# Kernel tuning notes

Measured on AMD Instinct MI355X. Metric: run time of the kernel, lower is better.

The kernel has to match this reference:

```python
import jax, jax.numpy as jnp
import numpy as np

NUM_HEAD = 8
HEAD_DIM = 64
TEMPERATURE = 10000.0


def positional_encoding(L, D):
    # Mirrors get_positional_encoding: sin on even-indexed, cos on odd-indexed
    # columns of pos, interleaved via stack+reshape.
    embed = jnp.arange(L, dtype=jnp.float32)
    dim_t = jnp.arange(D, dtype=jnp.float32)
    dim_t = TEMPERATURE ** (2.0 * jnp.floor(dim_t / 2.0) / D)
    pos = embed[:, None] / dim_t                      # [L, D]
    pos = jnp.stack([jnp.sin(pos[:, 0::2]), jnp.cos(pos[:, 1::2])], axis=2)
    return pos.reshape(1, L, D)                       # [1, L, D]


def setup_inputs() -> dict:
    key = jax.random.key(0)
    ks = jax.random.split(key, 4)
    B, L, D = 8, 1024, 256
    HD = NUM_HEAD * HEAD_DIM                          # 512
    glorot = float(np.sqrt(2.0 / (D + HD)))
    return {
        "x": jax.random.normal(ks[0], (B, L, D), jnp.float32),
        "Wq": jax.random.normal(ks[1], (D, HD), jnp.float32) * glorot,
        "bq": jnp.zeros((NUM_HEAD,), jnp.float32),
        "Wk": jax.random.normal(ks[2], (D, HD), jnp.float32) * glorot,
        "bk": jnp.zeros((NUM_HEAD,), jnp.float32),
        "Wv": jax.random.normal(ks[3], (D, HD), jnp.float32) * glorot,
        "bv": jnp.zeros((NUM_HEAD,), jnp.float32),
    }


def reference(x, Wq, bq, Wk, bk, Wv, bv):
    B, L, D = x.shape
    pe = positional_encoding(L, D)
    qk_in = x + pe                                    # query/key get pos-enc, value does not
    # per-head bias broadcast over head_dim (tf.repeat(bias, head_dim))
    q = qk_in @ Wq + jnp.repeat(bq, HEAD_DIM)
    k = qk_in @ Wk + jnp.repeat(bk, HEAD_DIM)
    v = x @ Wv + jnp.repeat(bv, HEAD_DIM)
    split = lambda t: t.reshape(B, L, NUM_HEAD, HEAD_DIM)
    q, k, v = split(q), split(k), split(v)
    att = jnp.einsum('blhd,bmhd->bhlm', q, k) * (float(HEAD_DIM) ** -0.5)
    att = jax.nn.softmax(att, axis=-1)                # [B, H, L, L]
    out = jnp.einsum('bhlm,bmhd->blhd', att, v)       # [B, L, H, hd]
    return out.reshape(B, L, NUM_HEAD * HEAD_DIM)
```

## Files before the change

kernel.cpp:

```cpp
#include <hip/hip_runtime.h>
#include <hip/hip_bf16.h>

#define NB   8
#define NL   1024
#define ND   256
#define NH   8
#define NHD  64
#define NC   512
#define NTOK (NB*NL)

typedef __bf16 bf16x8v __attribute__((ext_vector_type(8)));
typedef float f32x4 __attribute__((ext_vector_type(4)));

__device__ __forceinline__ unsigned short f2bf(float f) {
  unsigned u = __float_as_uint(f);
  unsigned r = (u + 0x7fffu + ((u >> 16) & 1u)) >> 16;
  return (unsigned short)r;
}

__device__ __forceinline__ unsigned pack_bf16x2(float lo, float hi) {
  __hip_bfloat162 h2 = __float22bfloat162_rn(make_float2(lo, hi));
  union { __hip_bfloat162 h; unsigned u; } cvt;
  cvt.h = h2;
  return cvt.u;
}

__global__ __launch_bounds__(256) void prep_kernel(
    const float* __restrict__ x,
    const float* __restrict__ Wq, const float* __restrict__ Wk,
    const float* __restrict__ Wv,
    unsigned short* __restrict__ xpe, unsigned short* __restrict__ xb,
    unsigned short* __restrict__ wqt, unsigned short* __restrict__ wkt,
    unsigned short* __restrict__ wvt) {
  const int bid = blockIdx.x;
  const int tid = threadIdx.x;
  if (bid < (NTOK * ND) / (256 * 8)) {
    int idx = bid * 256 + tid;
    int d0 = (idx & 31) * 8;
    int t = idx >> 5;
    int l = t & (NL - 1);
    float4 xa = *(const float4*)(x + (size_t)t * ND + d0);
    float4 xc = *(const float4*)(x + (size_t)t * ND + d0 + 4);
    float xv[8] = {xa.x, xa.y, xa.z, xa.w, xc.x, xc.y, xc.z, xc.w};
    unsigned short pe_out[8], xb_out[8];
#pragma unroll
    for (int p = 0; p < 4; ++p) {
      float inv_dim = __expf(-0.07195578415606394f * (float)(d0 / 2 + p));
      float ang = (float)l * inv_dim;
      float sv = __sinf(ang);
      float cv = __cosf(ang);
      pe_out[2 * p]     = f2bf(xv[2 * p] + sv);
      pe_out[2 * p + 1] = f2bf(xv[2 * p + 1] + cv);
      xb_out[2 * p]     = f2bf(xv[2 * p]);
      xb_out[2 * p + 1] = f2bf(xv[2 * p + 1]);
    }
    *(int4*)(xpe + (size_t)t * ND + d0) = *(int4*)pe_out;
    *(int4*)(xb  + (size_t)t * ND + d0) = *(int4*)xb_out;
  } else {
    __shared__ float tile[64 * 65];
    int widx = bid - (NTOK * ND) / (256 * 8);
    int m = widx >> 5;
    int tl = widx & 31;
    int kt = tl & 3;
    int nt = tl >> 2;
    const float* W = (m == 0) ? Wq : (m == 1) ? Wk : Wv;
    unsigned short* Wt = (m == 0) ? wqt : (m == 1) ? wkt : wvt;
    int c = tid & 63, rb = tid >> 6;
#pragma unroll
    for (int i = 0; i < 16; ++i) {
      int r = i * 4 + rb;
      tile[r * 65 + c] = W[(kt * 64 + r) * NC + nt * 64 + c];
    }
    __syncthreads();
#pragma unroll
    for (int i = 0; i < 16; ++i) {
      int n_local = i * 4 + rb, k_local = c;
      Wt[(nt * 64 + n_local) * ND + kt * 64 + k_local] =
          f2bf(tile[k_local * 65 + n_local]);
    }
  }
}

__global__ __launch_bounds__(256) void gemm_qkv_kernel(
    const unsigned short* __restrict__ xpe, const unsigned short* __restrict__ xb,
    const unsigned short* __restrict__ wqt, const unsigned short* __restrict__ wkt,
    const unsigned short* __restrict__ wvt,
    const float* __restrict__ bq, const float* __restrict__ bk,
    const float* __restrict__ bv,
    unsigned short* __restrict__ qg, unsigned short* __restrict__ kg,
    unsigned short* __restrict__ vg) {
  __shared__ unsigned short As[128 * 72];
  __shared__ unsigned short Bs[128 * 72];

  const int z = blockIdx.z;
  const unsigned short* X  = (z == 2) ? xb : xpe;
  const unsigned short* Wt = (z == 0) ? wqt : (z == 1) ? wkt : wvt;
  const float* bias        = (z == 0) ? bq  : (z == 1) ? bk  : bv;
  unsigned short* Out      = (z == 0) ? qg  : (z == 1) ? kg  : vg;
  const float scale        = (z == 0) ? 0.18033688011112042f : 1.0f;

  const int nt = blockIdx.x;
  const int mt = blockIdx.y;
  const int tid = threadIdx.x;
  const int w = tid >> 6;
  const int wm = w >> 1, wn = w & 1;
  const int lane = tid & 63;
  const int lg = lane >> 4;
  const int lr = lane & 15;

  const int r0 = tid >> 3;
  const int c8o = (tid & 7) * 8;
  const unsigned short* Abase = X + (size_t)(mt * 128 + r0) * ND + c8o;
  const unsigned short* Bbase = Wt + (size_t)(nt * 128 + r0) * ND + c8o;
  unsigned short* Adst = As + r0 * 72 + c8o;
  unsigned short* Bdst = Bs + r0 * 72 + c8o;

  f32x4 acc[4][4] = {};
  int4 a0, a1, a2, a3, b0, b1, b2, b3;

#define GLOADS(kb)                                              \
  a0 = *(const int4*)(Abase + (kb) * 64);                       \
  a1 = *(const int4*)(Abase + (kb) * 64 + 32 * ND);             \
  a2 = *(const int4*)(Abase + (kb) * 64 + 64 * ND);             \
  a3 = *(const int4*)(Abase + (kb) * 64 + 96 * ND);             \
  b0 = *(const int4*)(Bbase + (kb) * 64);                       \
  b1 = *(const int4*)(Bbase + (kb) * 64 + 32 * ND);             \
  b2 = *(const int4*)(Bbase + (kb) * 64 + 64 * ND);             \
  b3 = *(const int4*)(Bbase + (kb) * 64 + 96 * ND);

  GLOADS(0)
#pragma unroll
  for (int kb = 0; kb < 4; ++kb) {
    if (kb) __syncthreads();
    *(int4*)(Adst)           = a0;
    *(int4*)(Adst + 32 * 72) = a1;
    *(int4*)(Adst + 64 * 72) = a2;
    *(int4*)(Adst + 96 * 72) = a3;
    *(int4*)(Bdst)           = b0;
    *(int4*)(Bdst + 32 * 72) = b1;
    *(int4*)(Bdst + 64 * 72) = b2;
    *(int4*)(Bdst + 96 * 72) = b3;
    if (kb == 0) { GLOADS(1) }
    else if (kb == 1) { GLOADS(2) }
    else if (kb == 2) { GLOADS(3) }
    __syncthreads();

#pragma unroll
    for (int kk = 0; kk < 2; ++kk) {
      bf16x8v a[4], b[4];
#pragma unroll
      for (int mi = 0; mi < 4; ++mi)
        a[mi] = *(const bf16x8v*)(As + (wm * 64 + mi * 16 + lr) * 72 + kk * 32 + lg * 8);
#pragma unroll
      for (int nj = 0; nj < 4; ++nj)
        b[nj] = *(const bf16x8v*)(Bs + (wn * 64 + nj * 16 + lr) * 72 + kk * 32 + lg * 8);
#pragma unroll
      for (int mi = 0; mi < 4; ++mi)
#pragma unroll
        for (int nj = 0; nj < 4; ++nj)
          acc[mi][nj] = __builtin_amdgcn_mfma_f32_16x16x32_bf16(
              a[mi], b[nj], acc[mi][nj], 0, 0, 0);
    }
  }
#undef GLOADS

  const float bval = bias[nt * 2 + wn];
  const int h = nt * 2 + wn;
#pragma unroll
  for (int mi = 0; mi < 4; ++mi) {
#pragma unroll
    for (int nj = 0; nj < 4; ++nj) {
#pragma unroll
      for (int j = 0; j < 4; ++j) {
        int r = mt * 128 + wm * 64 + mi * 16 + lg * 4 + j;
        int dd = nj * 16 + lr;
        int bb = r >> 10, lpos = r & (NL - 1);
        float val = (acc[mi][nj][j] + bval) * scale;
        if (z < 2)
          Out[((bb * NH + h) * NL + lpos) * NHD + dd] = f2bf(val);
        else
          Out[((bb * NH + h) * NHD + dd) * NL + lpos] = f2bf(val);
      }
    }
  }
}

__global__ __launch_bounds__(256) void attn_kernel(
    const unsigned short* __restrict__ Q,
    const unsigned short* __restrict__ K,
    const unsigned short* __restrict__ Vt,
    float* __restrict__ Out) {
  __shared__ unsigned short Ks[64 * 72];
  __shared__ unsigned short Vs[64 * 72];
  __shared__ unsigned short Ps[64 * 72];

  const int qt = blockIdx.x;
  const int bh = blockIdx.y;
  const int bb = bh >> 3, h = bh & 7;
  const int tid = threadIdx.x;
  const int w = tid >> 6;
  const int lane = tid & 63;
  const int lg = lane >> 4, lr = lane & 15;
  const int qrow0 = qt * 64 + w * 16;

  bf16x8v qf[2];
#pragma unroll
  for (int kk = 0; kk < 2; ++kk)
    qf[kk] = *(const bf16x8v*)(Q + ((size_t)bh * NL + qrow0 + lr) * NHD + kk * 32 + lg * 8);

  const int r0 = tid >> 3;
  const int c8o = (tid & 7) * 8;
  const unsigned short* kp0 = K + (size_t)bh * NL * NHD + r0 * NHD + c8o;
  const unsigned short* vp0 = Vt + ((size_t)bh * NHD + r0) * NL + c8o;
  unsigned short* kdst = Ks + r0 * 72 + c8o;
  unsigned short* vdst = Vs + r0 * 72 + c8o;

  float m_ = -1e30f, lsum = 0.0f;
  f32x4 o[4] = {};
  int4 ka, kc, va, vc;

#define KVLOADS(kv)                                             \
  ka = *(const int4*)(kp0 + (kv) * 64 * NHD);                   \
  kc = *(const int4*)(kp0 + (kv) * 64 * NHD + 32 * NHD);        \
  va = *(const int4*)(vp0 + (kv) * 64);                         \
  vc = *(const int4*)(vp0 + (kv) * 64 + 32 * NL);

  KVLOADS(0)
  for (int kv = 0; kv < 16; ++kv) {
    if (kv) __syncthreads();
    *(int4*)(kdst)           = ka;
    *(int4*)(kdst + 32 * 72) = kc;
    *(int4*)(vdst)           = va;
    *(int4*)(vdst + 32 * 72) = vc;
    if (kv < 15) { KVLOADS(kv + 1) }
    __syncthreads();

    f32x4 s[4] = {};
    __builtin_amdgcn_s_setprio(1);
#pragma unroll
    for (int kk = 0; kk < 2; ++kk) {
#pragma unroll
      for (int nb = 0; nb < 4; ++nb) {
        bf16x8v kf = *(const bf16x8v*)(Ks + (nb * 16 + lr) * 72 + kk * 32 + lg * 8);
        s[nb] = __builtin_amdgcn_mfma_f32_16x16x32_bf16(kf, qf[kk], s[nb], 0, 0, 0);
      }
    }
    __builtin_amdgcn_s_setprio(0);

    float tm;
    {
      float a0 = fmaxf(s[0][0], s[0][1]), a1 = fmaxf(s[0][2], s[0][3]);
      float a2 = fmaxf(s[1][0], s[1][1]), a3 = fmaxf(s[1][2], s[1][3]);
      float a4 = fmaxf(s[2][0], s[2][1]), a5 = fmaxf(s[2][2], s[2][3]);
      float a6 = fmaxf(s[3][0], s[3][1]), a7 = fmaxf(s[3][2], s[3][3]);
      float c0 = fmaxf(fmaxf(a0, a1), fmaxf(a2, a3));
      float c1 = fmaxf(fmaxf(a4, a5), fmaxf(a6, a7));
      tm = fmaxf(c0, c1);
    }
    tm = fmaxf(tm, __shfl_xor(tm, 16, 64));
    tm = fmaxf(tm, __shfl_xor(tm, 32, 64));
    if (__any(tm > m_ + 8.0f)) {
      float nm = fmaxf(m_, tm);
      float corr = exp2f(m_ - nm);
      m_ = nm;
      lsum *= corr;
#pragma unroll
      for (int db = 0; db < 4; ++db)
#pragma unroll
        for (int j = 0; j < 4; ++j) o[db][j] *= corr;
    }
#pragma unroll
    for (int nb = 0; nb < 4; ++nb)
#pragma unroll
      for (int j = 0; j < 4; ++j)
        s[nb][j] = exp2f(s[nb][j] - m_);
    float ts;
    {
      float a0 = s[0][0] + s[0][1], a1 = s[0][2] + s[0][3];
      float a2 = s[1][0] + s[1][1], a3 = s[1][2] + s[1][3];
      float a4 = s[2][0] + s[2][1], a5 = s[2][2] + s[2][3];
      float a6 = s[3][0] + s[3][1], a7 = s[3][2] + s[3][3];
      ts = ((a0 + a1) + (a2 + a3)) + ((a4 + a5) + (a6 + a7));
    }
    ts += __shfl_xor(ts, 16, 64);
    ts += __shfl_xor(ts, 32, 64);
    lsum += ts;

#pragma unroll
    for (int nb = 0; nb < 4; ++nb)
#pragma unroll
      for (int hh = 0; hh < 2; ++hh)
        *(unsigned*)(Ps + (w * 16 + lr) * 72 + nb * 16 + lg * 4 + 2 * hh) =
            pack_bf16x2(s[nb][2 * hh], s[nb][2 * hh + 1]);

    __builtin_amdgcn_s_setprio(1);
#pragma unroll
    for (int kk = 0; kk < 2; ++kk) {
      bf16x8v pf = *(const bf16x8v*)(Ps + (w * 16 + lr) * 72 + kk * 32 + lg * 8);
#pragma unroll
      for (int db = 0; db < 4; ++db) {
        bf16x8v vf = *(const bf16x8v*)(Vs + (db * 16 + lr) * 72 + kk * 32 + lg * 8);
        o[db] = __builtin_amdgcn_mfma_f32_16x16x32_bf16(vf, pf, o[db], 0, 0, 0);
      }
    }
    __builtin_amdgcn_s_setprio(0);
  }
#undef KVLOADS

  float inv = 1.0f / lsum;
  int q = qrow0 + lr;
#pragma unroll
  for (int db = 0; db < 4; ++db) {
    f32x4 ov;
#pragma unroll
    for (int j = 0; j < 4; ++j) ov[j] = o[db][j] * inv;
    *(f32x4*)(Out + (size_t)(bb * NL + q) * NC + h * NHD + db * 16 + lg * 4) = ov;
  }
}

extern "C" void kernel_launch(void* const* d_in, const int* in_sizes, int n_in,
                              void* d_out, int out_size, void* d_ws, size_t ws_size,
                              hipStream_t stream) {
  const float* x  = (const float*)d_in[0];
  const float* Wq = (const float*)d_in[1];
  const float* bq = (const float*)d_in[2];
  const float* Wk = (const float*)d_in[3];
  const float* bk = (const float*)d_in[4];
  const float* Wv = (const float*)d_in[5];
  const float* bv = (const float*)d_in[6];
  float* out = (float*)d_out;

  unsigned short* xpe = (unsigned short*)d_ws;
  unsigned short* xb  = xpe + (size_t)NTOK * ND;
  unsigned short* wqt = xb  + (size_t)NTOK * ND;
  unsigned short* wkt = wqt + (size_t)ND * NC;
  unsigned short* wvt = wkt + (size_t)ND * NC;
  unsigned short* qg  = wvt + (size_t)ND * NC;
  unsigned short* kg  = qg  + (size_t)NB * NH * NL * NHD;
  unsigned short* vg  = kg  + (size_t)NB * NH * NL * NHD;

  int prep_blocks = (NTOK * ND) / (256 * 8) + 96;
  prep_kernel<<<prep_blocks, 256, 0, stream>>>(x, Wq, Wk, Wv, xpe, xb, wqt, wkt, wvt);

  gemm_qkv_kernel<<<dim3(4, 64, 3), 256, 0, stream>>>(
      xpe, xb, wqt, wkt, wvt, bq, bk, bv, qg, kg, vg);

  attn_kernel<<<dim3(16, 64), 256, 0, stream>>>(qg, kg, vg, out);
}
```

Before: 137.9 us.

## Fuse input conversion, positional encoding and weight transpose into QKV GEMM

Removes the separate prep kernel. The QKV GEMM now reads fp32 x and W directly, adds the sin/cos positional encoding on the fly for Q and K, converts to bf16, and transposes the weight tile into shared memory itself. This drops one launch and the bf16 intermediate round trip through global memory. In exchange the GEMM loses its register prefetch of the next k-block, recomputes the PE transcendentals in every N-tile block, and reads fp32 data at twice the width. The change also XOR-swizzles the LDS layouts of As, Bs, Ks, Vs and Ps to reduce bank conflicts.

After: 134.5 us. 1.03x faster.

```diff
diff --git a/kernel.cpp b/kernel.cpp
--- a/kernel.cpp
+++ b/kernel.cpp
@@ -25,66 +25,10 @@
   return cvt.u;
 }
 
-__global__ __launch_bounds__(256) void prep_kernel(
+__global__ __launch_bounds__(256) void gemm_qkv_fused_kernel(
     const float* __restrict__ x,
     const float* __restrict__ Wq, const float* __restrict__ Wk,
     const float* __restrict__ Wv,
-    unsigned short* __restrict__ xpe, unsigned short* __restrict__ xb,
-    unsigned short* __restrict__ wqt, unsigned short* __restrict__ wkt,
-    unsigned short* __restrict__ wvt) {
-  const int bid = blockIdx.x;
-  const int tid = threadIdx.x;
-  if (bid < (NTOK * ND) / (256 * 8)) {
-    int idx = bid * 256 + tid;
-    int d0 = (idx & 31) * 8;
-    int t = idx >> 5;
-    int l = t & (NL - 1);
-    float4 xa = *(const float4*)(x + (size_t)t * ND + d0);
-    float4 xc = *(const float4*)(x + (size_t)t * ND + d0 + 4);
-    float xv[8] = {xa.x, xa.y, xa.z, xa.w, xc.x, xc.y, xc.z, xc.w};
-    unsigned short pe_out[8], xb_out[8];
-#pragma unroll
-    for (int p = 0; p < 4; ++p) {
-      float inv_dim = __expf(-0.07195578415606394f * (float)(d0 / 2 + p));
-      float ang = (float)l * inv_dim;
-      float sv = __sinf(ang);
-      float cv = __cosf(ang);
-      pe_out[2 * p]     = f2bf(xv[2 * p] + sv);
-      pe_out[2 * p + 1] = f2bf(xv[2 * p + 1] + cv);
-      xb_out[2 * p]     = f2bf(xv[2 * p]);
-      xb_out[2 * p + 1] = f2bf(xv[2 * p + 1]);
-    }
-    *(int4*)(xpe + (size_t)t * ND + d0) = *(int4*)pe_out;
-    *(int4*)(xb  + (size_t)t * ND + d0) = *(int4*)xb_out;
-  } else {
-    __shared__ float tile[64 * 65];
-    int widx = bid - (NTOK * ND) / (256 * 8);
-    int m = widx >> 5;
-    int tl = widx & 31;
-    int kt = tl & 3;
-    int nt = tl >> 2;
-    const float* W = (m == 0) ? Wq : (m == 1) ? Wk : Wv;
-    unsigned short* Wt = (m == 0) ? wqt : (m == 1) ? wkt : wvt;
-    int c = tid & 63, rb = tid >> 6;
-#pragma unroll
-    for (int i = 0; i < 16; ++i) {
-      int r = i * 4 + rb;
-      tile[r * 65 + c] = W[(kt * 64 + r) * NC + nt * 64 + c];
-    }
-    __syncthreads();
-#pragma unroll
-    for (int i = 0; i < 16; ++i) {
-      int n_local = i * 4 + rb, k_local = c;
-      Wt[(nt * 64 + n_local) * ND + kt * 64 + k_local] =
-          f2bf(tile[k_local * 65 + n_local]);
-    }
-  }
-}
-
-__global__ __launch_bounds__(256) void gemm_qkv_kernel(
-    const unsigned short* __restrict__ xpe, const unsigned short* __restrict__ xb,
-    const unsigned short* __restrict__ wqt, const unsigned short* __restrict__ wkt,
-    const unsigned short* __restrict__ wvt,
     const float* __restrict__ bq, const float* __restrict__ bk,
     const float* __restrict__ bv,
     unsigned short* __restrict__ qg, unsigned short* __restrict__ kg,
@@ -93,11 +37,11 @@
   __shared__ unsigned short Bs[128 * 72];
 
   const int z = blockIdx.z;
-  const unsigned short* X  = (z == 2) ? xb : xpe;
-  const unsigned short* Wt = (z == 0) ? wqt : (z == 1) ? wkt : wvt;
-  const float* bias        = (z == 0) ? bq  : (z == 1) ? bk  : bv;
-  unsigned short* Out      = (z == 0) ? qg  : (z == 1) ? kg  : vg;
-  const float scale        = (z == 0) ? 0.18033688011112042f : 1.0f;
+  const float* Wsrc = (z == 0) ? Wq : (z == 1) ? Wk : Wv;
+  const float* bias = (z == 0) ? bq : (z == 1) ? bk : bv;
+  unsigned short* Out = (z == 0) ? qg : (z == 1) ? kg : vg;
+  const float scale = (z == 0) ? 0.18033688011112042f : 1.0f;
+  const bool addpe = (z < 2);
 
   const int nt = blockIdx.x;
   const int mt = blockIdx.y;
@@ -105,55 +49,83 @@
   const int w = tid >> 6;
   const int wm = w >> 1, wn = w & 1;
   const int lane = tid & 63;
-  const int lg = lane >> 4;
-  const int lr = lane & 15;
-
-  const int r0 = tid >> 3;
-  const int c8o = (tid & 7) * 8;
-  const unsigned short* Abase = X + (size_t)(mt * 128 + r0) * ND + c8o;
-  const unsigned short* Bbase = Wt + (size_t)(nt * 128 + r0) * ND + c8o;
-  unsigned short* Adst = As + r0 * 72 + c8o;
-  unsigned short* Bdst = Bs + r0 * 72 + c8o;
+  const int lg = lane >> 4, lr = lane & 15;
+
+  const int r0 = tid >> 3, c8 = tid & 7;
+  unsigned short* Adst = As + r0 * 72 + 8 * ((c8 + 2 * (r0 & 7)) & 7);
+  const float* xbase = x + (size_t)(mt * 128 + r0) * ND + c8 * 8;
+  const int no = tid & 15, kp0 = tid >> 4;
 
   f32x4 acc[4][4] = {};
-  int4 a0, a1, a2, a3, b0, b1, b2, b3;
-
-#define GLOADS(kb)                                              \
-  a0 = *(const int4*)(Abase + (kb) * 64);                       \
-  a1 = *(const int4*)(Abase + (kb) * 64 + 32 * ND);             \
-  a2 = *(const int4*)(Abase + (kb) * 64 + 64 * ND);             \
-  a3 = *(const int4*)(Abase + (kb) * 64 + 96 * ND);             \
-  b0 = *(const int4*)(Bbase + (kb) * 64);                       \
-  b1 = *(const int4*)(Bbase + (kb) * 64 + 32 * ND);             \
-  b2 = *(const int4*)(Bbase + (kb) * 64 + 64 * ND);             \
-  b3 = *(const int4*)(Bbase + (kb) * 64 + 96 * ND);
-
-  GLOADS(0)
-#pragma unroll
+
   for (int kb = 0; kb < 4; ++kb) {
     if (kb) __syncthreads();
-    *(int4*)(Adst)           = a0;
-    *(int4*)(Adst + 32 * 72) = a1;
-    *(int4*)(Adst + 64 * 72) = a2;
-    *(int4*)(Adst + 96 * 72) = a3;
-    *(int4*)(Bdst)           = b0;
-    *(int4*)(Bdst + 32 * 72) = b1;
-    *(int4*)(Bdst + 64 * 72) = b2;
-    *(int4*)(Bdst + 96 * 72) = b3;
-    if (kb == 0) { GLOADS(1) }
-    else if (kb == 1) { GLOADS(2) }
-    else if (kb == 2) { GLOADS(3) }
+    float i0 = 0.f, i1 = 0.f, i2 = 0.f, i3 = 0.f;
+    if (addpe) {
+      int dh = kb * 32 + c8 * 4;
+      i0 = __expf(-0.07195578415606394f * (float)(dh));
+      i1 = __expf(-0.07195578415606394f * (float)(dh + 1));
+      i2 = __expf(-0.07195578415606394f * (float)(dh + 2));
+      i3 = __expf(-0.07195578415606394f * (float)(dh + 3));
+    }
+#pragma unroll
+    for (int i = 0; i < 4; ++i) {
+      int row = r0 + 32 * i;
+      f32x4 xa = *(const f32x4*)(xbase + (size_t)(32 * i) * ND + kb * 64);
+      f32x4 xc = *(const f32x4*)(xbase + (size_t)(32 * i) * ND + kb * 64 + 4);
+      unsigned p0, p1, p2, p3;
+      if (addpe) {
+        float l = (float)((mt * 128 + row) & (NL - 1));
+        float a0 = l * i0, a1 = l * i1, a2 = l * i2, a3 = l * i3;
+        p0 = pack_bf16x2(xa[0] + __sinf(a0), xa[1] + __cosf(a0));
+        p1 = pack_bf16x2(xa[2] + __sinf(a1), xa[3] + __cosf(a1));
+        p2 = pack_bf16x2(xc[0] + __sinf(a2), xc[1] + __cosf(a2));
+        p3 = pack_bf16x2(xc[2] + __sinf(a3), xc[3] + __cosf(a3));
+      } else {
+        p0 = pack_bf16x2(xa[0], xa[1]);
+        p1 = pack_bf16x2(xa[2], xa[3]);
+        p2 = pack_bf16x2(xc[0], xc[1]);
+        p3 = pack_bf16x2(xc[2], xc[3]);
+      }
+      int4 pv; pv.x = (int)p0; pv.y = (int)p1; pv.z = (int)p2; pv.w = (int)p3;
+      *(int4*)(Adst + (size_t)(32 * i) * 72) = pv;
+    }
+#pragma unroll
+    for (int u = 0; u < 2; ++u) {
+      int kp = kp0 + 16 * u;
+      int krow = kb * 64 + 2 * kp;
+      const float* wr0 = Wsrc + (size_t)krow * NC + nt * 128 + no * 8;
+      const float* wr1 = wr0 + NC;
+      f32x4 w0a = *(const f32x4*)(wr0);
+      f32x4 w0b = *(const f32x4*)(wr0 + 4);
+      f32x4 w1a = *(const f32x4*)(wr1);
+      f32x4 w1b = *(const f32x4*)(wr1 + 4);
+#pragma unroll
+      for (int e = 0; e < 8; ++e) {
+        float lo = (e < 4) ? w0a[e] : w0b[e - 4];
+        float hi = (e < 4) ? w1a[e] : w1b[e - 4];
+        int n = no * 8 + e;
+        *(unsigned*)(Bs + n * 72 + 8 * (((kp >> 2) + (no & 7)) & 7) +
+                     (kp & 3) * 2) = pack_bf16x2(lo, hi);
+      }
+    }
     __syncthreads();
 
 #pragma unroll
     for (int kk = 0; kk < 2; ++kk) {
       bf16x8v a[4], b[4];
 #pragma unroll
-      for (int mi = 0; mi < 4; ++mi)
-        a[mi] = *(const bf16x8v*)(As + (wm * 64 + mi * 16 + lr) * 72 + kk * 32 + lg * 8);
-#pragma unroll
-      for (int nj = 0; nj < 4; ++nj)
-        b[nj] = *(const bf16x8v*)(Bs + (wn * 64 + nj * 16 + lr) * 72 + kk * 32 + lg * 8);
+      for (int mi = 0; mi < 4; ++mi) {
+        int row = wm * 64 + mi * 16 + lr;
+        a[mi] = *(const bf16x8v*)(As + row * 72 +
+                                  8 * ((4 * kk + lg + 2 * (row & 7)) & 7));
+      }
+#pragma unroll
+      for (int nj = 0; nj < 4; ++nj) {
+        int n = wn * 64 + nj * 16 + lr;
+        b[nj] = *(const bf16x8v*)(Bs + n * 72 +
+                                  8 * ((4 * kk + lg + ((n >> 3) & 7)) & 7));
+      }
 #pragma unroll
       for (int mi = 0; mi < 4; ++mi)
 #pragma unroll
@@ -162,7 +134,6 @@
               a[mi], b[nj], acc[mi][nj], 0, 0, 0);
     }
   }
-#undef GLOADS
 
   const float bval = bias[nt * 2 + wn];
   const int h = nt * 2 + wn;
@@ -209,11 +180,12 @@
     qf[kk] = *(const bf16x8v*)(Q + ((size_t)bh * NL + qrow0 + lr) * NHD + kk * 32 + lg * 8);
 
   const int r0 = tid >> 3;
-  const int c8o = (tid & 7) * 8;
-  const unsigned short* kp0 = K + (size_t)bh * NL * NHD + r0 * NHD + c8o;
-  const unsigned short* vp0 = Vt + ((size_t)bh * NHD + r0) * NL + c8o;
-  unsigned short* kdst = Ks + r0 * 72 + c8o;
-  unsigned short* vdst = Vs + r0 * 72 + c8o;
+  const int c8 = tid & 7;
+  const unsigned short* kp0 = K + (size_t)bh * NL * NHD + r0 * NHD + c8 * 8;
+  const unsigned short* vp0 = Vt + ((size_t)bh * NHD + r0) * NL + c8 * 8;
+  const int sw_st = 8 * ((c8 + 2 * (r0 & 7)) & 7);
+  unsigned short* kdst = Ks + r0 * 72 + sw_st;
+  unsigned short* vdst = Vs + r0 * 72 + sw_st;
 
   float m_ = -1e30f, lsum = 0.0f;
   f32x4 o[4] = {};
@@ -241,7 +213,9 @@
     for (int kk = 0; kk < 2; ++kk) {
 #pragma unroll
       for (int nb = 0; nb < 4; ++nb) {
-        bf16x8v kf = *(const bf16x8v*)(Ks + (nb * 16 + lr) * 72 + kk * 32 + lg * 8);
+        int row = nb * 16 + lr;
+        bf16x8v kf = *(const bf16x8v*)(Ks + row * 72 +
+                                       8 * ((4 * kk + lg + 2 * (row & 7)) & 7));
         s[nb] = __builtin_amdgcn_mfma_f32_16x16x32_bf16(kf, qf[kk], s[nb], 0, 0, 0);
       }
     }
@@ -286,20 +260,31 @@
     ts += __shfl_xor(ts, 32, 64);
     lsum += ts;
 
-#pragma unroll
-    for (int nb = 0; nb < 4; ++nb)
-#pragma unroll
-      for (int hh = 0; hh < 2; ++hh)
-        *(unsigned*)(Ps + (w * 16 + lr) * 72 + nb * 16 + lg * 4 + 2 * hh) =
-            pack_bf16x2(s[nb][2 * hh], s[nb][2 * hh + 1]);
+    {
+      int prow = w * 16 + lr;
+      unsigned short* pbase = Ps + prow * 72;
+      int key = 2 * (lr & 7);
+#pragma unroll
+      for (int nb = 0; nb < 4; ++nb)
+#pragma unroll
+        for (int hh = 0; hh < 2; ++hh) {
+          int slot = 2 * nb + (lg >> 1);
+          *(unsigned*)(pbase + 8 * ((slot + key) & 7) + (lg & 1) * 4 + 2 * hh) =
+              pack_bf16x2(s[nb][2 * hh], s[nb][2 * hh + 1]);
+        }
+    }
 
     __builtin_amdgcn_s_setprio(1);
 #pragma unroll
     for (int kk = 0; kk < 2; ++kk) {
-      bf16x8v pf = *(const bf16x8v*)(Ps + (w * 16 + lr) * 72 + kk * 32 + lg * 8);
+      int prow = w * 16 + lr;
+      bf16x8v pf = *(const bf16x8v*)(Ps + prow * 72 +
+                                     8 * ((4 * kk + lg + 2 * (lr & 7)) & 7));
 #pragma unroll
       for (int db = 0; db < 4; ++db) {
-        bf16x8v vf = *(const bf16x8v*)(Vs + (db * 16 + lr) * 72 + kk * 32 + lg * 8);
+        int row = db * 16 + lr;
+        bf16x8v vf = *(const bf16x8v*)(Vs + row * 72 +
+                                       8 * ((4 * kk + lg + 2 * (row & 7)) & 7));
         o[db] = __builtin_amdgcn_mfma_f32_16x16x32_bf16(vf, pf, o[db], 0, 0, 0);
       }
     }
@@ -330,20 +315,12 @@
   const float* bv = (const float*)d_in[6];
   float* out = (float*)d_out;
 
-  unsigned short* xpe = (unsigned short*)d_ws;
-  unsigned short* xb  = xpe + (size_t)NTOK * ND;
-  unsigned short* wqt = xb  + (size_t)NTOK * ND;
-  unsigned short* wkt = wqt + (size_t)ND * NC;
-  unsigned short* wvt = wkt + (size_t)ND * NC;
-  unsigned short* qg  = wvt + (size_t)ND * NC;
-  unsigned short* kg  = qg  + (size_t)NB * NH * NL * NHD;
-  unsigned short* vg  = kg  + (size_t)NB * NH * NL * NHD;
-
-  int prep_blocks = (NTOK * ND) / (256 * 8) + 96;
-  prep_kernel<<<prep_blocks, 256, 0, stream>>>(x, Wq, Wk, Wv, xpe, xb, wqt, wkt, wvt);
-
-  gemm_qkv_kernel<<<dim3(4, 64, 3), 256, 0, stream>>>(
-      xpe, xb, wqt, wkt, wvt, bq, bk, bv, qg, kg, vg);
+  unsigned short* qg = (unsigned short*)d_ws;
+  unsigned short* kg = qg + (size_t)NB * NH * NL * NHD;
+  unsigned short* vg = kg + (size_t)NB * NH * NL * NHD;
+
+  gemm_qkv_fused_kernel<<<dim3(4, 64, 3), 256, 0, stream>>>(
+      x, Wq, Wk, Wv, bq, bk, bv, qg, kg, vg);
 
   attn_kernel<<<dim3(16, 64), 256, 0, stream>>>(qg, kg, vg, out);
 }
```
